# Kernel tuning notes

Measured on AMD Instinct MI355X. Metric: run time of the kernel, lower is better.

The kernel has to match this reference:

```python
import jax, jax.numpy as jnp
import numpy as np

B, L, D = 4, 4096, 1024
H = 16
DK = D // H  # 64
EPS = 1e-5


def setup_inputs() -> dict:
    key = jax.random.key(0)
    ks = jax.random.split(key, 9)
    s = 1.0 / np.sqrt(D)
    return {
        "Q": jax.random.normal(ks[0], (B, L, D), dtype=jnp.float32),
        "W_Q": jax.random.uniform(ks[1], (D, D), jnp.float32, -s, s),
        "b_Q": jax.random.uniform(ks[2], (D,), jnp.float32, -s, s),
        "W_K": jax.random.uniform(ks[3], (D, D), jnp.float32, -s, s),
        "b_K": jax.random.uniform(ks[4], (D,), jnp.float32, -s, s),
        "W_V": jax.random.uniform(ks[5], (D, D), jnp.float32, -s, s),
        "b_V": jax.random.uniform(ks[6], (D,), jnp.float32, -s, s),
        "W_O": jax.random.uniform(ks[7], (D, D), jnp.float32, -s, s),
        "b_O": jax.random.uniform(ks[8], (D,), jnp.float32, -s, s),
    }


def reference(Q, W_Q, b_Q, W_K, b_K, W_V, b_V, W_O, b_O):
    # Projections (torch Linear: x @ W.T + b). K = V = Q (self-attention).
    q = (Q @ W_Q.T + b_Q).reshape(B, L, H, DK)  # blhd
    k = (Q @ W_K.T + b_K).reshape(B, L, H, DK)
    v = (Q @ W_V.T + b_V).reshape(B, L, H, DK)

    phi_q = jax.nn.elu(q) + 1.0
    phi_k = jax.nn.elu(k) + 1.0

    # KV outer-product accumulation over sequence: [b,h,d,m]
    KV = jnp.einsum('blhd,blhm->bhdm', phi_k, v)
    K_sum = phi_k.sum(axis=1)                       # [b,h,d]
    Z = 1.0 / (jnp.einsum('blhd,bhd->blh', phi_q, K_sum) + EPS)
    V_new = jnp.einsum('blhd,bhdm->blhm', phi_q, KV) * Z[..., None]

    out = V_new.reshape(B, L, H * DK) @ W_O.T + b_O  # [b,L,d_model]
    return out
```

## Files before the change

### kernel.cpp

```cpp
#include <hip/hip_runtime.h>

typedef unsigned short u16;
typedef unsigned int   u32;
typedef __attribute__((ext_vector_type(8))) short short8;
typedef __attribute__((ext_vector_type(4))) float f32x4;
typedef __attribute__((ext_vector_type(4))) u16   u16x4;

#define NB 4
#define SL 4096
#define DM 1024
#define NH 16
#define DK 64

__device__ __forceinline__ u16 f2bf(float f) {
  u32 u = __builtin_bit_cast(u32, f);
  u = (u + 0x7fffu + ((u >> 16) & 1u)) >> 16;
  return (u16)u;
}
__device__ __forceinline__ float bf2f(u16 v) {
  u32 u = ((u32)v) << 16;
  return __builtin_bit_cast(float, u);
}
__device__ __forceinline__ float eluP1(float x) {
  return x > 0.f ? x + 1.f : __expf(x);
}
__device__ __forceinline__ void gll16(const u16* g, u16* l) {
  __builtin_amdgcn_global_load_lds((const __attribute__((address_space(1))) void*)g,
                                   (__attribute__((address_space(3))) void*)l, 16, 0, 0);
}

__global__ void cvt_f32_bf16(const float* __restrict__ in, u16* __restrict__ out, int n4) {
  int i = blockIdx.x * 256 + threadIdx.x;
  if (i < n4) {
    f32x4 f = *(const f32x4*)(in + (size_t)i * 4);
    u16x4 o = { f2bf(f[0]), f2bf(f[1]), f2bf(f[2]), f2bf(f[3]) };
    *(u16x4*)(out + (size_t)i * 4) = o;
  }
}

__global__ void cvt_w(const float* __restrict__ WQ, const float* __restrict__ WK,
                      const float* __restrict__ WV, const float* __restrict__ WO,
                      u16* __restrict__ Wqkv, u16* __restrict__ Wobf) {
  int r = blockIdx.x >> 10;
  int i = (blockIdx.x & 1023) * 256 + threadIdx.x;
  const float* src = r == 0 ? WQ : r == 1 ? WK : r == 2 ? WV : WO;
  u16* dst = (r == 3) ? Wobf : Wqkv + (size_t)r * 1048576;
  f32x4 f = *(const f32x4*)(src + (size_t)i * 4);
  u16x4 o = { f2bf(f[0]), f2bf(f[1]), f2bf(f[2]), f2bf(f[3]) };
  *(u16x4*)(dst + (size_t)i * 4) = o;
}

__global__ void pack_bias(const float* __restrict__ bQ, const float* __restrict__ bK,
                          const float* __restrict__ bV, float* __restrict__ biasQKV) {
  int i = blockIdx.x * 256 + threadIdx.x;
  float v = (i < 1024) ? bQ[i] : (i < 2048) ? bK[i - 1024] : bV[i - 2048];
  biasQKV[i] = v;
}

__global__ __launch_bounds__(256) void gemm_qkv(const u16* __restrict__ A,
                                                const u16* __restrict__ Wqkv,
                                                const float* __restrict__ biasQKV,
                                                u16* __restrict__ phiq,
                                                u16* __restrict__ phiKT,
                                                u16* __restrict__ vT) {
  const int K = 1024;
  const int bId = blockIdx.x;
  const int xcd = bId & 7, s = bId >> 3;
  const int xm = xcd >> 1, xn = xcd & 1;
  const int tm_l = s / 12, tn_l = s - tm_l * 12;
  const int tile_m = xm * 32 + tm_l;
  const int tile_n = xn * 12 + tn_l;
  const int region = tile_n >> 3;

  const int tid = threadIdx.x, lane = tid & 63, wv = tid >> 6;
  const int i16 = lane & 15, q = lane >> 4;
  const int waveR = wv >> 1, waveC = wv & 1;

  __shared__ u16 Xs[128 * 32];
  __shared__ u16 Ws[128 * 32];

  const int rbase = wv * 32 + (lane >> 2);
  const int kc = (lane & 3) ^ ((rbase >> 1) & 3);
  const u16* Ag = A + (size_t)(tile_m * 128 + rbase) * K + kc * 8;
  const u16* Wg = Wqkv + (size_t)(tile_n * 128 + rbase) * K + kc * 8;
  u16* XsB = Xs + wv * 1024;
  u16* WsB = Ws + wv * 1024;

  f32x4 acc[4][4] = {};

  const u16* aT = (region == 0) ? Ws : Xs;
  const u16* bT = (region == 0) ? Xs : Ws;

  for (int k0 = 0; k0 < K; k0 += 32) {
    __syncthreads();
    gll16(Ag + k0,          XsB);
    gll16(Ag + k0 + 16 * K, XsB + 512);
    gll16(Wg + k0,          WsB);
    gll16(Wg + k0 + 16 * K, WsB + 512);
    __syncthreads();

    short8 af[4], bfr[4];
#pragma unroll
    for (int t = 0; t < 4; t++) {
      int m = waveR * 64 + t * 16 + i16;
      af[t] = *(const short8*)(aT + m * 32 + ((q ^ ((m >> 1) & 3)) << 3));
    }
#pragma unroll
    for (int u = 0; u < 4; u++) {
      int m = waveC * 64 + u * 16 + i16;
      bfr[u] = *(const short8*)(bT + m * 32 + ((q ^ ((m >> 1) & 3)) << 3));
    }
#pragma unroll
    for (int t = 0; t < 4; t++)
#pragma unroll
      for (int u = 0; u < 4; u++)
        acc[t][u] = __builtin_amdgcn_mfma_f32_16x16x32_bf16(af[t], bfr[u], acc[t][u], 0, 0, 0);
  }

  if (region == 0) {
#pragma unroll
    for (int t = 0; t < 4; t++) {
#pragma unroll
      for (int u = 0; u < 4; u++) {
        int n_glb = tile_n * 128 + waveR * 64 + t * 16 + q * 4;
        int m_glb = tile_m * 128 + waveC * 64 + u * 16 + i16;
        f32x4 b4 = *(const f32x4*)(biasQKV + n_glb);
        u16x4 o;
#pragma unroll
        for (int r = 0; r < 4; r++) o[r] = f2bf(eluP1(acc[t][u][r] + b4[r]));
        *(u16x4*)(phiq + (size_t)m_glb * DM + n_glb) = o;
      }
    }
  } else {
    u16* dst = (region == 1) ? phiKT : vT;
    const bool act = (region == 1);
#pragma unroll
    for (int t = 0; t < 4; t++) {
#pragma unroll
      for (int u = 0; u < 4; u++) {
        int n_row = tile_n * 128 + waveC * 64 + u * 16 + i16;
        int n_loc = n_row - region * 1024;
        int m_row = tile_m * 128 + waveR * 64 + t * 16 + q * 4;
        int bI = m_row >> 12, l = m_row & 4095;
        float bsc = biasQKV[n_row];
        u16x4 o;
#pragma unroll
        for (int r = 0; r < 4; r++) {
          float vv = acc[t][u][r] + bsc;
          if (act) vv = eluP1(vv);
          o[r] = f2bf(vv);
        }
        *(u16x4*)(dst + (size_t)bI * (DM * SL) + (size_t)n_loc * SL + l) = o;
      }
    }
  }
}

__global__ __launch_bounds__(256) void gemm_out(const u16* __restrict__ A,
                                                const u16* __restrict__ W,
                                                const float* __restrict__ bias,
                                                float* __restrict__ outp) {
  const int K = 1024;
  const int bId = blockIdx.x;
  const int xcd = bId & 7, s = bId >> 3;
  const int xm = xcd >> 1, xn = xcd & 1;
  const int tm_l = s >> 2, tn_l = s & 3;
  const int tile_m = xm * 32 + tm_l;
  const int tile_n = xn * 4 + tn_l;

  const int tid = threadIdx.x, lane = tid & 63, wv = tid >> 6;
  const int i16 = lane & 15, q = lane >> 4;
  const int waveR = wv >> 1, waveC = wv & 1;

  __shared__ u16 Xs[128 * 32];
  __shared__ u16 Ws[128 * 32];

  const int rbase = wv * 32 + (lane >> 2);
  const int kc = (lane & 3) ^ ((rbase >> 1) & 3);
  const u16* Ag = A + (size_t)(tile_m * 128 + rbase) * K + kc * 8;
  const u16* Wg = W + (size_t)(tile_n * 128 + rbase) * K + kc * 8;
  u16* XsB = Xs + wv * 1024;
  u16* WsB = Ws + wv * 1024;

  f32x4 acc[4][4] = {};

  for (int k0 = 0; k0 < K; k0 += 32) {
    __syncthreads();
    gll16(Ag + k0,          XsB);
    gll16(Ag + k0 + 16 * K, XsB + 512);
    gll16(Wg + k0,          WsB);
    gll16(Wg + k0 + 16 * K, WsB + 512);
    __syncthreads();

    short8 af[4], bfr[4];
#pragma unroll
    for (int t = 0; t < 4; t++) {
      int m = waveR * 64 + t * 16 + i16;
      af[t] = *(const short8*)(Ws + m * 32 + ((q ^ ((m >> 1) & 3)) << 3));
    }
#pragma unroll
    for (int u = 0; u < 4; u++) {
      int m = waveC * 64 + u * 16 + i16;
      bfr[u] = *(const short8*)(Xs + m * 32 + ((q ^ ((m >> 1) & 3)) << 3));
    }
#pragma unroll
    for (int t = 0; t < 4; t++)
#pragma unroll
      for (int u = 0; u < 4; u++)
        acc[t][u] = __builtin_amdgcn_mfma_f32_16x16x32_bf16(af[t], bfr[u], acc[t][u], 0, 0, 0);
  }

#pragma unroll
  for (int t = 0; t < 4; t++) {
#pragma unroll
    for (int u = 0; u < 4; u++) {
      int n_glb = tile_n * 128 + waveR * 64 + t * 16 + q * 4;
      int m_glb = tile_m * 128 + waveC * 64 + u * 16 + i16;
      f32x4 b4 = *(const f32x4*)(bias + n_glb);
      f32x4 o;
#pragma unroll
      for (int r = 0; r < 4; r++) o[r] = acc[t][u][r] + b4[r];
      *(f32x4*)(outp + (size_t)m_glb * DM + n_glb) = o;
    }
  }
}

__global__ __launch_bounds__(256) void kv_partial(const u16* __restrict__ phiKT,
                                                  const u16* __restrict__ vT,
                                                  float* __restrict__ part,
                                                  float* __restrict__ ksumP) {
  int bh = blockIdx.x >> 2, chunk = blockIdx.x & 3;
  int tid = threadIdx.x, lane = tid & 63, wv = tid >> 6;
  int i16 = lane & 15, q = lane >> 4;
  const u16* Ab = phiKT + (size_t)bh * DK * SL;
  const u16* Bb = vT + (size_t)bh * DK * SL;
  int l0 = (chunk * 4 + wv) * 256;
  f32x4 acc[4][4] = {};
  float ks[4] = {};
  for (int kk = 0; kk < 256; kk += 32) {
    int col = l0 + kk + q * 8;
    short8 af[4], bfr[4];
#pragma unroll
    for (int t = 0; t < 4; t++) af[t] = *(const short8*)(Ab + (size_t)(t * 16 + i16) * SL + col);
#pragma unroll
    for (int u = 0; u < 4; u++) bfr[u] = *(const short8*)(Bb + (size_t)(u * 16 + i16) * SL + col);
#pragma unroll
    for (int t = 0; t < 4; t++)
#pragma unroll
      for (int j = 0; j < 8; j++) ks[t] += bf2f((u16)af[t][j]);
#pragma unroll
    for (int t = 0; t < 4; t++)
#pragma unroll
      for (int u = 0; u < 4; u++)
        acc[t][u] = __builtin_amdgcn_mfma_f32_16x16x32_bf16(af[t], bfr[u], acc[t][u], 0, 0, 0);
  }
  __shared__ float red[4][64][64];
  __shared__ float ksl[4][4][64];
#pragma unroll
  for (int t = 0; t < 4; t++)
#pragma unroll
    for (int u = 0; u < 4; u++)
#pragma unroll
      for (int r = 0; r < 4; r++)
        red[wv][t * 16 + q * 4 + r][u * 16 + i16] = acc[t][u][r];
#pragma unroll
  for (int t = 0; t < 4; t++) ksl[wv][q][t * 16 + i16] = ks[t];
  __syncthreads();
  int d = tid >> 2, mg = (tid & 3) * 16;
  for (int mm = 0; mm < 16; mm++) {
    int m = mg + mm;
    float s = red[0][d][m] + red[1][d][m] + red[2][d][m] + red[3][d][m];
    part[((size_t)(chunk * 64 + bh) * 64 + d) * 64 + m] = s;
  }
  if (tid < 64) {
    float s = 0.f;
#pragma unroll
    for (int w2 = 0; w2 < 4; w2++)
#pragma unroll
      for (int q2 = 0; q2 < 4; q2++) s += ksl[w2][q2][tid];
    ksumP[chunk * 4096 + bh * 64 + tid] = s;
  }
}

__global__ __launch_bounds__(256) void kv_finalize(const float* __restrict__ part,
                                                   const float* __restrict__ ksumP,
                                                   u16* __restrict__ KVt,
                                                   float* __restrict__ Ksum) {
  int bh = blockIdx.x, tid = threadIdx.x;
  for (int e = tid; e < 4096; e += 256) {
    int d = e >> 6, m = e & 63;
    float s = part[((size_t)(0 * 64 + bh) * 64 + d) * 64 + m]
            + part[((size_t)(1 * 64 + bh) * 64 + d) * 64 + m]
            + part[((size_t)(2 * 64 + bh) * 64 + d) * 64 + m]
            + part[((size_t)(3 * 64 + bh) * 64 + d) * 64 + m];
    KVt[(size_t)bh * 4096 + m * 64 + d] = f2bf(s);
  }
  if (tid < 64) {
    float s = ksumP[0 * 4096 + bh * 64 + tid] + ksumP[1 * 4096 + bh * 64 + tid]
            + ksumP[2 * 4096 + bh * 64 + tid] + ksumP[3 * 4096 + bh * 64 + tid];
    Ksum[bh * 64 + tid] = s;
  }
}

__global__ __launch_bounds__(256) void vnew_kernel(const u16* __restrict__ phiq,
                                                   const u16* __restrict__ KVt,
                                                   const float* __restrict__ Ksum,
                                                   u16* __restrict__ Vnew) {
  int bh = blockIdx.x >> 5, lt = blockIdx.x & 31;
  int b = bh >> 4, h = bh & 15;
  int tid = threadIdx.x, lane = tid & 63, wv = tid >> 6;
  int i16 = lane & 15, q = lane >> 4;
  int waveM = wv & 1, waveL = wv >> 1;

  __shared__ float Zs[128];
  __shared__ float Pp[128][2];
  {
    int l = tid >> 1, half = tid & 1;
    const u16* pr = phiq + (size_t)(b * SL + lt * 128 + l) * DM + h * 64 + half * 32;
    float s = 0.f;
    for (int i = 0; i < 32; i += 8) {
      short8 v8 = *(const short8*)(pr + i);
#pragma unroll
      for (int j = 0; j < 8; j++) s += bf2f((u16)v8[j]) * Ksum[bh * 64 + half * 32 + i + j];
    }
    Pp[l][half] = s;
  }
  __syncthreads();
  if (tid < 128) Zs[tid] = 1.0f / (Pp[tid][0] + Pp[tid][1] + 1e-5f);
  __syncthreads();

  f32x4 acc[2][4] = {};
#pragma unroll
  for (int step = 0; step < 2; step++) {
    int d0 = step * 32 + q * 8;
    short8 af[2], bfr[4];
#pragma unroll
    for (int t = 0; t < 2; t++) {
      int m = waveM * 32 + t * 16 + i16;
      af[t] = *(const short8*)(KVt + (size_t)bh * 4096 + m * 64 + d0);
    }
#pragma unroll
    for (int u = 0; u < 4; u++) {
      int l = lt * 128 + waveL * 64 + u * 16 + i16;
      bfr[u] = *(const short8*)(phiq + (size_t)(b * SL + l) * DM + h * 64 + d0);
    }
#pragma unroll
    for (int t = 0; t < 2; t++)
#pragma unroll
      for (int u = 0; u < 4; u++)
        acc[t][u] = __builtin_amdgcn_mfma_f32_16x16x32_bf16(af[t], bfr[u], acc[t][u], 0, 0, 0);
  }

#pragma unroll
  for (int t = 0; t < 2; t++) {
#pragma unroll
    for (int u = 0; u < 4; u++) {
      int l_loc = waveL * 64 + u * 16 + i16;
      float z = Zs[l_loc];
      int n = h * 64 + waveM * 32 + t * 16 + q * 4;
      u16x4 o;
#pragma unroll
      for (int r = 0; r < 4; r++) o[r] = f2bf(acc[t][u][r] * z);
      *(u16x4*)(Vnew + (size_t)(b * SL + lt * 128 + l_loc) * DM + n) = o;
    }
  }
}

extern "C" void kernel_launch(void* const* d_in, const int* in_sizes, int n_in,
                              void* d_out, int out_size, void* d_ws, size_t ws_size,
                              hipStream_t stream) {
  const float* Qf = (const float*)d_in[0];
  const float* WQ = (const float*)d_in[1];
  const float* bQ = (const float*)d_in[2];
  const float* WK = (const float*)d_in[3];
  const float* bK = (const float*)d_in[4];
  const float* WV = (const float*)d_in[5];
  const float* bV = (const float*)d_in[6];
  const float* WO = (const float*)d_in[7];
  const float* bO = (const float*)d_in[8];

  const size_t MB = 1024ull * 1024ull;
  char* ws = (char*)d_ws;
  u16* Qbf     = (u16*)(ws + 0);
  u16* Vnew    = (u16*)(ws + 0);
  u16* Wqkv    = (u16*)(ws + 32 * MB);
  u16* Wobf    = (u16*)(ws + 38 * MB);
  float* biasQKV = (float*)(ws + 40 * MB);
  u16* phiq    = (u16*)(ws + 41 * MB);
  u16* phiKT   = (u16*)(ws + 73 * MB);
  u16* vT      = (u16*)(ws + 105 * MB);
  u16* KVt     = (u16*)(ws + 137 * MB);
  float* Ksum  = (float*)(ws + 138 * MB);
  float* part  = (float*)(ws + 139 * MB);
  float* ksumP = (float*)(ws + 143 * MB);

  cvt_f32_bf16<<<16384, 256, 0, stream>>>(Qf, Qbf, 4194304);
  cvt_w<<<4096, 256, 0, stream>>>(WQ, WK, WV, WO, Wqkv, Wobf);
  pack_bias<<<12, 256, 0, stream>>>(bQ, bK, bV, biasQKV);

  gemm_qkv<<<3072, 256, 0, stream>>>(Qbf, Wqkv, biasQKV, phiq, phiKT, vT);

  kv_partial<<<256, 256, 0, stream>>>(phiKT, vT, part, ksumP);
  kv_finalize<<<64, 256, 0, stream>>>(part, ksumP, KVt, Ksum);

  vnew_kernel<<<2048, 256, 0, stream>>>(phiq, KVt, Ksum, Vnew);

  gemm_out<<<1024, 256, 0, stream>>>(Vnew, Wobf, bO, (float*)d_out);
}
```

Before: 383.5 us.

## Double-buffer GEMM LDS loads and stage epilogues through LDS for coalesced stores

Both projection GEMMs now prefetch the next K-slice into a second LDS buffer while computing the current one, which removes one barrier per iteration. Epilogues in gemm_qkv, gemm_out and vnew_kernel write tiles into padded shared memory and then issue row-contiguous 16-byte global stores, so outputs are coalesced instead of scattered 8-byte writes. The block-to-tile mapping is changed to group tiles per XCD along M, and kv_partial writes its partial sums as vector stores. In exchange, shared memory use rises, which may lower occupancy, and extra barriers are added in the epilogues.

```diff
diff --git a/kernel.cpp b/kernel.cpp
--- a/kernel.cpp
+++ b/kernel.cpp
@@ -66,38 +66,49 @@
   const int K = 1024;
   const int bId = blockIdx.x;
   const int xcd = bId & 7, s = bId >> 3;
-  const int xm = xcd >> 1, xn = xcd & 1;
-  const int tm_l = s / 12, tn_l = s - tm_l * 12;
-  const int tile_m = xm * 32 + tm_l;
-  const int tile_n = xn * 12 + tn_l;
+  const int tile_n = s >> 4;
+  const int tile_m = xcd * 16 + (s & 15);
   const int region = tile_n >> 3;
 
   const int tid = threadIdx.x, lane = tid & 63, wv = tid >> 6;
   const int i16 = lane & 15, q = lane >> 4;
   const int waveR = wv >> 1, waveC = wv & 1;
 
-  __shared__ u16 Xs[128 * 32];
-  __shared__ u16 Ws[128 * 32];
+  __shared__ u16 smem[17408];
 
   const int rbase = wv * 32 + (lane >> 2);
   const int kc = (lane & 3) ^ ((rbase >> 1) & 3);
   const u16* Ag = A + (size_t)(tile_m * 128 + rbase) * K + kc * 8;
   const u16* Wg = Wqkv + (size_t)(tile_n * 128 + rbase) * K + kc * 8;
-  u16* XsB = Xs + wv * 1024;
-  u16* WsB = Ws + wv * 1024;
 
   f32x4 acc[4][4] = {};
 
-  const u16* aT = (region == 0) ? Ws : Xs;
-  const u16* bT = (region == 0) ? Xs : Ws;
-
-  for (int k0 = 0; k0 < K; k0 += 32) {
+  {
+    u16* XsB = smem + wv * 1024;
+    u16* WsB = smem + 4096 + wv * 1024;
+    gll16(Ag, XsB);
+    gll16(Ag + 16 * K, XsB + 512);
+    gll16(Wg, WsB);
+    gll16(Wg + 16 * K, WsB + 512);
+  }
+
+  for (int k = 0; k < 32; k++) {
+    const int cur = k & 1;
     __syncthreads();
-    gll16(Ag + k0,          XsB);
-    gll16(Ag + k0 + 16 * K, XsB + 512);
-    gll16(Wg + k0,          WsB);
-    gll16(Wg + k0 + 16 * K, WsB + 512);
-    __syncthreads();
+    if (k < 31) {
+      const int nxt = cur ^ 1;
+      const int k0 = (k + 1) * 32;
+      u16* XsB = smem + nxt * 8192 + wv * 1024;
+      u16* WsB = smem + nxt * 8192 + 4096 + wv * 1024;
+      gll16(Ag + k0,          XsB);
+      gll16(Ag + k0 + 16 * K, XsB + 512);
+      gll16(Wg + k0,          WsB);
+      gll16(Wg + k0 + 16 * K, WsB + 512);
+    }
+    const u16* Xc = smem + cur * 8192;
+    const u16* Wc = Xc + 4096;
+    const u16* aT = (region == 0) ? Wc : Xc;
+    const u16* bT = (region == 0) ? Xc : Wc;
 
     short8 af[4], bfr[4];
 #pragma unroll
@@ -117,40 +128,46 @@
         acc[t][u] = __builtin_amdgcn_mfma_f32_16x16x32_bf16(af[t], bfr[u], acc[t][u], 0, 0, 0);
   }
 
-  if (region == 0) {
-#pragma unroll
-    for (int t = 0; t < 4; t++) {
-#pragma unroll
-      for (int u = 0; u < 4; u++) {
-        int n_glb = tile_n * 128 + waveR * 64 + t * 16 + q * 4;
-        int m_glb = tile_m * 128 + waveC * 64 + u * 16 + i16;
-        f32x4 b4 = *(const f32x4*)(biasQKV + n_glb);
-        u16x4 o;
+  __syncthreads();
+  u16* T = smem;
+#pragma unroll
+  for (int t = 0; t < 4; t++) {
+#pragma unroll
+    for (int u = 0; u < 4; u++) {
+      int cI = waveC * 64 + u * 16 + i16;
+      int rI = waveR * 64 + t * 16 + q * 4;
+      u16x4 o;
+      if (region == 0) {
+        f32x4 b4 = *(const f32x4*)(biasQKV + tile_n * 128 + rI);
 #pragma unroll
         for (int r = 0; r < 4; r++) o[r] = f2bf(eluP1(acc[t][u][r] + b4[r]));
-        *(u16x4*)(phiq + (size_t)m_glb * DM + n_glb) = o;
-      }
-    }
-  } else {
-    u16* dst = (region == 1) ? phiKT : vT;
-    const bool act = (region == 1);
-#pragma unroll
-    for (int t = 0; t < 4; t++) {
-#pragma unroll
-      for (int u = 0; u < 4; u++) {
-        int n_row = tile_n * 128 + waveC * 64 + u * 16 + i16;
-        int n_loc = n_row - region * 1024;
-        int m_row = tile_m * 128 + waveR * 64 + t * 16 + q * 4;
-        int bI = m_row >> 12, l = m_row & 4095;
-        float bsc = biasQKV[n_row];
-        u16x4 o;
+      } else {
+        float bs = biasQKV[tile_n * 128 + cI];
 #pragma unroll
         for (int r = 0; r < 4; r++) {
-          float vv = acc[t][u][r] + bsc;
-          if (act) vv = eluP1(vv);
+          float vv = acc[t][u][r] + bs;
+          if (region == 1) vv = eluP1(vv);
           o[r] = f2bf(vv);
         }
-        *(u16x4*)(dst + (size_t)bI * (DM * SL) + (size_t)n_loc * SL + l) = o;
+      }
+      *(u16x4*)(T + cI * 136 + rI) = o;
+    }
+  }
+  __syncthreads();
+  {
+    const int Rl = tid >> 4, j = tid & 15;
+    u16* dst = (region == 1) ? phiKT : vT;
+#pragma unroll
+    for (int p = 0; p < 8; p++) {
+      int R = p * 16 + Rl;
+      short8 v8 = *(const short8*)(T + R * 136 + j * 8);
+      if (region == 0) {
+        *(short8*)(phiq + (size_t)(tile_m * 128 + R) * DM + tile_n * 128 + j * 8) = v8;
+      } else {
+        int n_loc = tile_n * 128 + R - region * 1024;
+        int bI = tile_m >> 5;
+        int l = (tile_m & 31) * 128 + j * 8;
+        *(short8*)(dst + ((size_t)bI * 1024 + n_loc) * 4096 + l) = v8;
       }
     }
   }
@@ -163,45 +180,57 @@
   const int K = 1024;
   const int bId = blockIdx.x;
   const int xcd = bId & 7, s = bId >> 3;
-  const int xm = xcd >> 1, xn = xcd & 1;
-  const int tm_l = s >> 2, tn_l = s & 3;
-  const int tile_m = xm * 32 + tm_l;
-  const int tile_n = xn * 4 + tn_l;
+  const int tile_n = s >> 4;
+  const int tile_m = xcd * 16 + (s & 15);
 
   const int tid = threadIdx.x, lane = tid & 63, wv = tid >> 6;
   const int i16 = lane & 15, q = lane >> 4;
   const int waveR = wv >> 1, waveC = wv & 1;
 
-  __shared__ u16 Xs[128 * 32];
-  __shared__ u16 Ws[128 * 32];
+  __shared__ u16 smem[17408];
 
   const int rbase = wv * 32 + (lane >> 2);
   const int kc = (lane & 3) ^ ((rbase >> 1) & 3);
   const u16* Ag = A + (size_t)(tile_m * 128 + rbase) * K + kc * 8;
   const u16* Wg = W + (size_t)(tile_n * 128 + rbase) * K + kc * 8;
-  u16* XsB = Xs + wv * 1024;
-  u16* WsB = Ws + wv * 1024;
 
   f32x4 acc[4][4] = {};
 
-  for (int k0 = 0; k0 < K; k0 += 32) {
+  {
+    u16* XsB = smem + wv * 1024;
+    u16* WsB = smem + 4096 + wv * 1024;
+    gll16(Ag, XsB);
+    gll16(Ag + 16 * K, XsB + 512);
+    gll16(Wg, WsB);
+    gll16(Wg + 16 * K, WsB + 512);
+  }
+
+  for (int k = 0; k < 32; k++) {
+    const int cur = k & 1;
     __syncthreads();
-    gll16(Ag + k0,          XsB);
-    gll16(Ag + k0 + 16 * K, XsB + 512);
-    gll16(Wg + k0,          WsB);
-    gll16(Wg + k0 + 16 * K, WsB + 512);
-    __syncthreads();
+    if (k < 31) {
+      const int nxt = cur ^ 1;
+      const int k0 = (k + 1) * 32;
+      u16* XsB = smem + nxt * 8192 + wv * 1024;
+      u16* WsB = smem + nxt * 8192 + 4096 + wv * 1024;
+      gll16(Ag + k0,          XsB);
+      gll16(Ag + k0 + 16 * K, XsB + 512);
+      gll16(Wg + k0,          WsB);
+      gll16(Wg + k0 + 16 * K, WsB + 512);
+    }
+    const u16* Xc = smem + cur * 8192;
+    const u16* Wc = Xc + 4096;
 
     short8 af[4], bfr[4];
 #pragma unroll
     for (int t = 0; t < 4; t++) {
       int m = waveR * 64 + t * 16 + i16;
-      af[t] = *(const short8*)(Ws + m * 32 + ((q ^ ((m >> 1) & 3)) << 3));
+      af[t] = *(const short8*)(Wc + m * 32 + ((q ^ ((m >> 1) & 3)) << 3));
     }
 #pragma unroll
     for (int u = 0; u < 4; u++) {
       int m = waveC * 64 + u * 16 + i16;
-      bfr[u] = *(const short8*)(Xs + m * 32 + ((q ^ ((m >> 1) & 3)) << 3));
+      bfr[u] = *(const short8*)(Xc + m * 32 + ((q ^ ((m >> 1) & 3)) << 3));
     }
 #pragma unroll
     for (int t = 0; t < 4; t++)
@@ -210,17 +239,32 @@
         acc[t][u] = __builtin_amdgcn_mfma_f32_16x16x32_bf16(af[t], bfr[u], acc[t][u], 0, 0, 0);
   }
 
-#pragma unroll
-  for (int t = 0; t < 4; t++) {
-#pragma unroll
-    for (int u = 0; u < 4; u++) {
-      int n_glb = tile_n * 128 + waveR * 64 + t * 16 + q * 4;
-      int m_glb = tile_m * 128 + waveC * 64 + u * 16 + i16;
-      f32x4 b4 = *(const f32x4*)(bias + n_glb);
-      f32x4 o;
-#pragma unroll
-      for (int r = 0; r < 4; r++) o[r] = acc[t][u][r] + b4[r];
-      *(f32x4*)(outp + (size_t)m_glb * DM + n_glb) = o;
+  float* Tf = (float*)smem;
+#pragma unroll
+  for (int half = 0; half < 2; half++) {
+    __syncthreads();
+    if (waveR == half) {
+#pragma unroll
+      for (int t = 0; t < 4; t++) {
+#pragma unroll
+        for (int u = 0; u < 4; u++) {
+          int cI = waveC * 64 + u * 16 + i16;
+          int rIh = t * 16 + q * 4;
+          f32x4 b4 = *(const f32x4*)(bias + tile_n * 128 + half * 64 + rIh);
+          f32x4 o;
+#pragma unroll
+          for (int r = 0; r < 4; r++) o[r] = acc[t][u][r] + b4[r];
+          *(f32x4*)(Tf + cI * 68 + rIh) = o;
+        }
+      }
+    }
+    __syncthreads();
+    const int Rl = tid >> 4, j = tid & 15;
+#pragma unroll
+    for (int p = 0; p < 8; p++) {
+      int R = p * 16 + Rl;
+      f32x4 v = *(const f32x4*)(Tf + R * 68 + j * 4);
+      *(f32x4*)(outp + (size_t)(tile_m * 128 + R) * DM + tile_n * 128 + half * 64 + j * 4) = v;
     }
   }
 }
@@ -267,10 +311,14 @@
   for (int t = 0; t < 4; t++) ksl[wv][q][t * 16 + i16] = ks[t];
   __syncthreads();
   int d = tid >> 2, mg = (tid & 3) * 16;
-  for (int mm = 0; mm < 16; mm++) {
-    int m = mg + mm;
-    float s = red[0][d][m] + red[1][d][m] + red[2][d][m] + red[3][d][m];
-    part[((size_t)(chunk * 64 + bh) * 64 + d) * 64 + m] = s;
+#pragma unroll
+  for (int c = 0; c < 4; c++) {
+    int m = mg + c * 4;
+    f32x4 o;
+#pragma unroll
+    for (int r = 0; r < 4; r++)
+      o[r] = red[0][d][m + r] + red[1][d][m + r] + red[2][d][m + r] + red[3][d][m + r];
+    *(f32x4*)(part + ((size_t)(chunk * 64 + bh) * 64 + d) * 64 + m) = o;
   }
   if (tid < 64) {
     float s = 0.f;
@@ -314,6 +362,7 @@
 
   __shared__ float Zs[128];
   __shared__ float Pp[128][2];
+  __shared__ u16 T[128 * 72];
   {
     int l = tid >> 1, half = tid & 1;
     const u16* pr = phiq + (size_t)(b * SL + lt * 128 + l) * DM + h * 64 + half * 32;
@@ -355,13 +404,23 @@
   for (int t = 0; t < 2; t++) {
 #pragma unroll
     for (int u = 0; u < 4; u++) {
-      int l_loc = waveL * 64 + u * 16 + i16;
-      float z = Zs[l_loc];
-      int n = h * 64 + waveM * 32 + t * 16 + q * 4;
+      int cI = waveL * 64 + u * 16 + i16;
+      int nI = waveM * 32 + t * 16 + q * 4;
+      float z = Zs[cI];
       u16x4 o;
 #pragma unroll
       for (int r = 0; r < 4; r++) o[r] = f2bf(acc[t][u][r] * z);
-      *(u16x4*)(Vnew + (size_t)(b * SL + lt * 128 + l_loc) * DM + n) = o;
+      *(u16x4*)(T + cI * 72 + nI) = o;
+    }
+  }
+  __syncthreads();
+  {
+    const int Rl = tid >> 3, j = tid & 7;
+#pragma unroll
+    for (int p = 0; p < 4; p++) {
+      int R = p * 32 + Rl;
+      short8 v8 = *(const short8*)(T + R * 72 + j * 8);
+      *(short8*)(Vnew + (size_t)(b * SL + lt * 128 + R) * DM + h * 64 + j * 8) = v8;
     }
   }
 }
```

New measurement: 372.4 us. 2.9% less time.
